# Performance work log

Hardware: AMD Instinct MI355X
Metric: run time of the kernel (lower is better)

Reference implementation:

```python
import jax, jax.numpy as jnp
from jax import lax
import numpy as np

B = 1048576       # batched program states
L = 64            # hidden width of LinearNNComplex
STEPS = 19        # While test: state[5] < var(19), step counter +1 per iter


def setup_inputs() -> dict:
    key = jax.random.key(0)
    ks = jax.random.split(key, 7)
    x = jax.random.normal(ks[0], (B, 6), dtype=jnp.float32)
    x = x.at[:, 5].set(0.0)  # step counter starts at 0 so the While runs 19 iters
    # LinearNNComplex params: Linear(2,L) -> ReLU -> Linear(L,L) -> ReLU -> Linear(L,3) -> Sigmoid
    s1 = 1.0 / np.sqrt(2.0)
    s2 = 1.0 / np.sqrt(float(L))
    W1 = jax.random.normal(ks[1], (2, L), dtype=jnp.float32) * s1
    b1 = jax.random.normal(ks[2], (L,), dtype=jnp.float32) * s1
    W2 = jax.random.normal(ks[3], (L, L), dtype=jnp.float32) * s2
    b2 = jax.random.normal(ks[4], (L,), dtype=jnp.float32) * s2
    W3 = jax.random.normal(ks[5], (L, 3), dtype=jnp.float32) * s2
    b3 = jax.random.normal(ks[6], (3,), dtype=jnp.float32) * s2
    return {"x": x, "W1": W1, "b1": b1, "W2": W2, "b2": b2, "W3": W3, "b3": b3}


def reference(x, W1, b1, W2, b2, W3, b3):
    """Batched Program interpreter.

    State columns: [0]=position, [1]=forward counter, [2:5]=branch probs,
    [5]=step counter. Each iteration:
      state[2:5] = sigmoid-MLP(state[0:2])            (assign_branch_probability)
      argmax over cols 2,3,4 picks branch:            (argmax_p)
        0 -> move_up    (col0 -= 1)
        1 -> move_right (col0 unchanged)
        2 -> move_down  (col0 += 1)
      state[1] += 1                                   (forward_update)
      state[5] += 1                                   (step_update)
    Runs STEPS=19 iterations (While: state[5] < 19).
    """
    def nn(z):  # z: [B, 2]
        h = jax.nn.relu(z @ W1 + b1)
        h = jax.nn.relu(h @ W2 + b2)
        return jax.nn.sigmoid(h @ W3 + b3)  # [B, 3]

    def body(state, _):
        p = nn(state[:, :2])                         # [B, 3]
        idx = jnp.argmax(p, axis=-1)                 # [B]
        delta = (idx - 1).astype(state.dtype)        # up=-1, right=0, down=+1
        new = jnp.concatenate(
            [
                (state[:, 0] + delta)[:, None],
                (state[:, 1] + 1.0)[:, None],
                p,
                (state[:, 5] + 1.0)[:, None],
            ],
            axis=-1,
        )
        return new, None

    final, _ = lax.scan(body, x, None, length=STEPS)
    return final  # [B, 6]
```

## Files before the change

kernel.cpp:

```cpp
#include <hip/hip_runtime.h>
#include <math.h>


#define NSTEPS 19

typedef _Float16 half8   __attribute__((ext_vector_type(8)));
typedef _Float16 half2v  __attribute__((ext_vector_type(2)));
typedef float    float2v __attribute__((ext_vector_type(2)));
typedef float    float4v __attribute__((ext_vector_type(4)));

__device__ __forceinline__ half2v pkrtz(float a, float b) {
    return __builtin_bit_cast(half2v, __builtin_amdgcn_cvt_pkrtz(a, b));
}
__device__ __forceinline__ float swz_xor16(float v) {
    int r = __builtin_amdgcn_ds_swizzle(__builtin_bit_cast(int, v), 0x401F);
    return __builtin_bit_cast(float, r);
}
__device__ __forceinline__ float2v lo2(float4v v) {
    return __builtin_shufflevector(v, v, 0, 1);
}
__device__ __forceinline__ float2v hi2(float4v v) {
    return __builtin_shufflevector(v, v, 2, 3);
}

__global__ __launch_bounds__(256, 2)
void program_kernel(const float* __restrict__ x,
                    const float* __restrict__ W1,
                    const float* __restrict__ b1,
                    const float* __restrict__ W2,
                    const float* __restrict__ b2,
                    const float* __restrict__ W3,
                    const float* __restrict__ b3,
                    float* __restrict__ out,
                    int B) {
    const int tid    = threadIdx.x;
    const int lane   = tid & 63;
    const int wave   = tid >> 6;
    const int lanelo = lane & 15;
    const int q8     = lane >> 4;
    const int myRow  = blockIdx.x * 64 + wave * 16 + lanelo;
    const int rowLd  = myRow < B ? myRow : (B - 1);

    float2v w1a[8], w1b[8], b1v[8];
    #pragma unroll
    for (int kf = 0; kf < 2; ++kf) {
        const int k0 = kf * 32 + q8 * 8;
        const float2v* a = (const float2v*)(W1 + k0);
        const float2v* bb = (const float2v*)(W1 + 64 + k0);
        const float2v* bv = (const float2v*)(b1 + k0);
        #pragma unroll
        for (int i = 0; i < 4; ++i) {
            w1a[kf * 4 + i] = a[i];
            w1b[kf * 4 + i] = bb[i];
            b1v[kf * 4 + i] = bv[i];
        }
    }

    half8 Wh[2][4], Wl[2][4];
    #pragma unroll
    for (int kf = 0; kf < 2; ++kf) {
        #pragma unroll
        for (int t = 0; t < 4; ++t) {
            half8 bh, bl;
            #pragma unroll
            for (int j = 0; j < 8; ++j) {
                const float w =
                    W2[(kf * 32 + q8 * 8 + j) * 64 + t * 16 + lanelo];
                const _Float16 wh = (_Float16)w;
                const _Float16 wl = (_Float16)((w - (float)wh) * 4096.0f);
                bh[j] = wh;
                bl[j] = wl;
            }
            Wh[kf][t] = bh;
            Wl[kf][t] = bl;
        }
    }

    float4v b2f[4];
    #pragma unroll
    for (int t = 0; t < 4; ++t) {
        const int n = t * 16 + q8 * 4;
        b2f[t] = (float4v){b2[n], b2[n + 1], b2[n + 2], b2[n + 3]};
    }

    float2v d10[8], d20[8];
    #pragma unroll
    for (int p = 0; p < 8; ++p) {
        const int n0 = (p >> 1) * 16 + q8 * 4 + (p & 1) * 2;
        const float w00 = W3[n0 * 3 + 0],       w01 = W3[n0 * 3 + 1];
        const float w02 = W3[n0 * 3 + 2];
        const float w10 = W3[(n0 + 1) * 3 + 0], w11 = W3[(n0 + 1) * 3 + 1];
        const float w12 = W3[(n0 + 1) * 3 + 2];
        d10[p] = (float2v){w01 - w00, w11 - w10};
        d20[p] = (float2v){w02 - w00, w12 - w10};
    }
    const float b3v0 = b3[0];
    const float db10 = b3[1] - b3[0];
    const float db20 = b3[2] - b3[0];

    float pos, fwd, c5;
    {
        const float* xr = x + (size_t)rowLd * 6;
        pos = xr[0];
        fwd = xr[1];
        c5  = xr[5];
    }

    const float4v zf = {0.f, 0.f, 0.f, 0.f};
    const float2v z2 = {0.f, 0.f};
    const float2v kinv = {1.0f / 4096.0f, 1.0f / 4096.0f};
    float l0 = 0.f, l1 = 0.f, l2 = 0.f;

    #pragma unroll 1
    for (int step = 0; step < NSTEPS; ++step) {
        const float2v posp = {pos, pos}, fwdp = {fwd, fwd};
        half8 Hh[2], Hl[2];
        #pragma unroll
        for (int kf = 0; kf < 2; ++kf) {
            union { half8 v; half2v h2[4]; } uh, ul;
            #pragma unroll
            for (int p = 0; p < 4; ++p) {
                const int e = kf * 4 + p;
                float2v z = __builtin_elementwise_fma(fwdp, w1b[e], b1v[e]);
                z = __builtin_elementwise_fma(posp, w1a[e], z);
                const float2v hp = __builtin_elementwise_max(z, z2);
                uh.h2[p] = pkrtz(hp[0], hp[1]);
                const float r0 = fmaf((float)uh.h2[p][0], -1.0f, hp[0]);
                const float r1 = fmaf((float)uh.h2[p][1], -1.0f, hp[1]);
                const float2v rp = (float2v){r0, r1} * 4096.0f;
                ul.h2[p] = pkrtz(rp[0], rp[1]);
            }
            Hh[kf] = uh.v;
            Hl[kf] = ul.v;
        }

        float4v accA[4], accB[4];
        #pragma unroll
        for (int t = 0; t < 4; ++t) {
            accB[t] = __builtin_amdgcn_mfma_f32_16x16x32_f16(
                Wl[0][t], Hh[0], zf, 0, 0, 0);
            accB[t] = __builtin_amdgcn_mfma_f32_16x16x32_f16(
                Wh[0][t], Hl[0], accB[t], 0, 0, 0);
            accB[t] = __builtin_amdgcn_mfma_f32_16x16x32_f16(
                Wl[1][t], Hh[1], accB[t], 0, 0, 0);
            accB[t] = __builtin_amdgcn_mfma_f32_16x16x32_f16(
                Wh[1][t], Hl[1], accB[t], 0, 0, 0);
            accA[t] = __builtin_amdgcn_mfma_f32_16x16x32_f16(
                Wh[0][t], Hh[0], b2f[t], 0, 0, 0);
            accA[t] = __builtin_amdgcn_mfma_f32_16x16x32_f16(
                Wh[1][t], Hh[1], accA[t], 0, 0, 0);
        }

        float2v h2p[8];
        #pragma unroll
        for (int t = 0; t < 4; ++t) {
            h2p[2 * t] = __builtin_elementwise_max(
                __builtin_elementwise_fma(lo2(accB[t]), kinv, lo2(accA[t])),
                z2);
            h2p[2 * t + 1] = __builtin_elementwise_max(
                __builtin_elementwise_fma(hi2(accB[t]), kinv, hi2(accA[t])),
                z2);
        }

        float2v s1 = z2, s2 = z2;
        #pragma unroll
        for (int p = 0; p < 8; ++p) {
            s1 = __builtin_elementwise_fma(h2p[p], d10[p], s1);
            s2 = __builtin_elementwise_fma(h2p[p], d20[p], s2);
        }
        float g10 = s1[0] + s1[1];
        float g20 = s2[0] + s2[1];
        g10 += swz_xor16(g10);
        g20 += swz_xor16(g20);
        g10 += __shfl_xor(g10, 32, 64);
        g20 += __shfl_xor(g20, 32, 64);
        g10 += db10;
        g20 += db20;

        if (step == NSTEPS - 1) {
            float2v s0 = z2;
            #pragma unroll
            for (int p = 0; p < 8; ++p) {
                const int n0 = (p >> 1) * 16 + q8 * 4 + (p & 1) * 2;
                const float2v w30 = {W3[n0 * 3], W3[(n0 + 1) * 3]};
                s0 = __builtin_elementwise_fma(h2p[p], w30, s0);
            }
            float t0 = s0[0] + s0[1];
            t0 += swz_xor16(t0);
            t0 += __shfl_xor(t0, 32, 64);
            l0 = t0 + b3v0;
            l1 = l0 + g10;
            l2 = l0 + g20;
        }

        const float delta =
            (g20 > fmaxf(0.f, g10)) ? 1.0f : ((g10 > 0.f) ? 0.0f : -1.0f);
        pos += delta;
        fwd += 1.0f;
    }

    if (q8 == 0 && myRow < B) {
        const float p0 = 1.f / (1.f + __expf(-l0));
        const float p1 = 1.f / (1.f + __expf(-l1));
        const float p2 = 1.f / (1.f + __expf(-l2));
        float2* o = (float2*)(out + (size_t)myRow * 6);
        o[0] = make_float2(pos, fwd);
        o[1] = make_float2(p0, p1);
        o[2] = make_float2(p2, c5 + (float)NSTEPS);
    }
}

extern "C" void kernel_launch(void* const* d_in, const int* in_sizes, int n_in,
                              void* d_out, int out_size, void* d_ws, size_t ws_size,
                              hipStream_t stream) {
    const float* x  = (const float*)d_in[0];
    const float* W1 = (const float*)d_in[1];
    const float* b1 = (const float*)d_in[2];
    const float* W2 = (const float*)d_in[3];
    const float* b2 = (const float*)d_in[4];
    const float* W3 = (const float*)d_in[5];
    const float* b3 = (const float*)d_in[6];
    float* out = (float*)d_out;

    const int B = in_sizes[0] / 6;
    const int nBlocks = (B + 63) / 64;

    program_kernel<<<nBlocks, 256, 0, stream>>>(
        x, W1, b1, W2, b2, W3, b3, out, B);
}
```

Baseline: 632.6 us.

## Process three 16-row tiles per wave to amortize register-resident weights

Each wave now handles three independent 16-row sub-tiles instead of one, reusing the register-held split-fp16 W2 fragments and layer-1/layer-3 constants across them. Blocks shrink to a single wave and the grid is resized. This cuts the per-row cost of the weight setup and gives the scheduler independent MFMA chains to interleave. In exchange it raises register pressure, which may lower occupancy, and it changes the block shape.

Result: slower. 801.8 us (+26.7%).

```diff
diff --git a/kernel.cpp b/kernel.cpp
--- a/kernel.cpp
+++ b/kernel.cpp
@@ -3,6 +3,7 @@
 
 
 #define NSTEPS 19
+#define NS 3
 
 typedef _Float16 half8   __attribute__((ext_vector_type(8)));
 typedef _Float16 half2v  __attribute__((ext_vector_type(2)));
@@ -23,7 +24,7 @@
     return __builtin_shufflevector(v, v, 2, 3);
 }
 
-__global__ __launch_bounds__(256, 2)
+__global__ __launch_bounds__(64, 1)
 void program_kernel(const float* __restrict__ x,
                     const float* __restrict__ W1,
                     const float* __restrict__ b1,
@@ -33,13 +34,16 @@
                     const float* __restrict__ b3,
                     float* __restrict__ out,
                     int B) {
-    const int tid    = threadIdx.x;
-    const int lane   = tid & 63;
-    const int wave   = tid >> 6;
+    const int lane   = threadIdx.x & 63;
     const int lanelo = lane & 15;
     const int q8     = lane >> 4;
-    const int myRow  = blockIdx.x * 64 + wave * 16 + lanelo;
-    const int rowLd  = myRow < B ? myRow : (B - 1);
+
+    int myRow[NS], rowLd[NS];
+    #pragma unroll
+    for (int S = 0; S < NS; ++S) {
+        myRow[S] = blockIdx.x * (16 * NS) + S * 16 + lanelo;
+        rowLd[S] = myRow[S] < B ? myRow[S] : (B - 1);
+    }
 
     float2v w1a[8], w1b[8], b1v[8];
     #pragma unroll
@@ -98,115 +102,132 @@
     const float db10 = b3[1] - b3[0];
     const float db20 = b3[2] - b3[0];
 
-    float pos, fwd, c5;
-    {
-        const float* xr = x + (size_t)rowLd * 6;
-        pos = xr[0];
-        fwd = xr[1];
-        c5  = xr[5];
+    float pos[NS], fwd[NS], c5[NS];
+    #pragma unroll
+    for (int S = 0; S < NS; ++S) {
+        const float* xr = x + (size_t)rowLd[S] * 6;
+        pos[S] = xr[0];
+        fwd[S] = xr[1];
+        c5[S]  = xr[5];
     }
 
     const float4v zf = {0.f, 0.f, 0.f, 0.f};
     const float2v z2 = {0.f, 0.f};
     const float2v kinv = {1.0f / 4096.0f, 1.0f / 4096.0f};
-    float l0 = 0.f, l1 = 0.f, l2 = 0.f;
+    float l0[NS], l1[NS], l2[NS];
+    #pragma unroll
+    for (int S = 0; S < NS; ++S) { l0[S] = l1[S] = l2[S] = 0.f; }
 
     #pragma unroll 1
     for (int step = 0; step < NSTEPS; ++step) {
-        const float2v posp = {pos, pos}, fwdp = {fwd, fwd};
-        half8 Hh[2], Hl[2];
-        #pragma unroll
-        for (int kf = 0; kf < 2; ++kf) {
-            union { half8 v; half2v h2[4]; } uh, ul;
-            #pragma unroll
-            for (int p = 0; p < 4; ++p) {
-                const int e = kf * 4 + p;
-                float2v z = __builtin_elementwise_fma(fwdp, w1b[e], b1v[e]);
-                z = __builtin_elementwise_fma(posp, w1a[e], z);
-                const float2v hp = __builtin_elementwise_max(z, z2);
-                uh.h2[p] = pkrtz(hp[0], hp[1]);
-                const float r0 = fmaf((float)uh.h2[p][0], -1.0f, hp[0]);
-                const float r1 = fmaf((float)uh.h2[p][1], -1.0f, hp[1]);
-                const float2v rp = (float2v){r0, r1} * 4096.0f;
-                ul.h2[p] = pkrtz(rp[0], rp[1]);
-            }
-            Hh[kf] = uh.v;
-            Hl[kf] = ul.v;
-        }
-
-        float4v accA[4], accB[4];
-        #pragma unroll
-        for (int t = 0; t < 4; ++t) {
-            accB[t] = __builtin_amdgcn_mfma_f32_16x16x32_f16(
-                Wl[0][t], Hh[0], zf, 0, 0, 0);
-            accB[t] = __builtin_amdgcn_mfma_f32_16x16x32_f16(
-                Wh[0][t], Hl[0], accB[t], 0, 0, 0);
-            accB[t] = __builtin_amdgcn_mfma_f32_16x16x32_f16(
-                Wl[1][t], Hh[1], accB[t], 0, 0, 0);
-            accB[t] = __builtin_amdgcn_mfma_f32_16x16x32_f16(
-                Wh[1][t], Hl[1], accB[t], 0, 0, 0);
-            accA[t] = __builtin_amdgcn_mfma_f32_16x16x32_f16(
-                Wh[0][t], Hh[0], b2f[t], 0, 0, 0);
-            accA[t] = __builtin_amdgcn_mfma_f32_16x16x32_f16(
-                Wh[1][t], Hh[1], accA[t], 0, 0, 0);
-        }
-
-        float2v h2p[8];
-        #pragma unroll
-        for (int t = 0; t < 4; ++t) {
-            h2p[2 * t] = __builtin_elementwise_max(
-                __builtin_elementwise_fma(lo2(accB[t]), kinv, lo2(accA[t])),
-                z2);
-            h2p[2 * t + 1] = __builtin_elementwise_max(
-                __builtin_elementwise_fma(hi2(accB[t]), kinv, hi2(accA[t])),
-                z2);
-        }
-
-        float2v s1 = z2, s2 = z2;
-        #pragma unroll
-        for (int p = 0; p < 8; ++p) {
-            s1 = __builtin_elementwise_fma(h2p[p], d10[p], s1);
-            s2 = __builtin_elementwise_fma(h2p[p], d20[p], s2);
-        }
-        float g10 = s1[0] + s1[1];
-        float g20 = s2[0] + s2[1];
-        g10 += swz_xor16(g10);
-        g20 += swz_xor16(g20);
-        g10 += __shfl_xor(g10, 32, 64);
-        g20 += __shfl_xor(g20, 32, 64);
-        g10 += db10;
-        g20 += db20;
-
-        if (step == NSTEPS - 1) {
-            float2v s0 = z2;
+        half8 Hh[NS][2], Hl[NS][2];
+        #pragma unroll
+        for (int S = 0; S < NS; ++S) {
+            const float2v posp = {pos[S], pos[S]}, fwdp = {fwd[S], fwd[S]};
+            #pragma unroll
+            for (int kf = 0; kf < 2; ++kf) {
+                union { half8 v; half2v h2[4]; } uh, ul;
+                #pragma unroll
+                for (int p = 0; p < 4; ++p) {
+                    const int e = kf * 4 + p;
+                    float2v z = __builtin_elementwise_fma(fwdp, w1b[e], b1v[e]);
+                    z = __builtin_elementwise_fma(posp, w1a[e], z);
+                    const float2v hp = __builtin_elementwise_max(z, z2);
+                    uh.h2[p] = pkrtz(hp[0], hp[1]);
+                    const float r0 = fmaf((float)uh.h2[p][0], -1.0f, hp[0]);
+                    const float r1 = fmaf((float)uh.h2[p][1], -1.0f, hp[1]);
+                    const float2v rp = (float2v){r0, r1} * 4096.0f;
+                    ul.h2[p] = pkrtz(rp[0], rp[1]);
+                }
+                Hh[S][kf] = uh.v;
+                Hl[S][kf] = ul.v;
+            }
+        }
+
+        float4v accA[NS][4], accB[NS][4];
+        #pragma unroll
+        for (int S = 0; S < NS; ++S) {
+            #pragma unroll
+            for (int t = 0; t < 4; ++t) {
+                accB[S][t] = __builtin_amdgcn_mfma_f32_16x16x32_f16(
+                    Wl[0][t], Hh[S][0], zf, 0, 0, 0);
+                accB[S][t] = __builtin_amdgcn_mfma_f32_16x16x32_f16(
+                    Wh[0][t], Hl[S][0], accB[S][t], 0, 0, 0);
+                accB[S][t] = __builtin_amdgcn_mfma_f32_16x16x32_f16(
+                    Wl[1][t], Hh[S][1], accB[S][t], 0, 0, 0);
+                accB[S][t] = __builtin_amdgcn_mfma_f32_16x16x32_f16(
+                    Wh[1][t], Hl[S][1], accB[S][t], 0, 0, 0);
+                accA[S][t] = __builtin_amdgcn_mfma_f32_16x16x32_f16(
+                    Wh[0][t], Hh[S][0], b2f[t], 0, 0, 0);
+                accA[S][t] = __builtin_amdgcn_mfma_f32_16x16x32_f16(
+                    Wh[1][t], Hh[S][1], accA[S][t], 0, 0, 0);
+            }
+        }
+
+        #pragma unroll
+        for (int S = 0; S < NS; ++S) {
+            float2v h2p[8];
+            #pragma unroll
+            for (int t = 0; t < 4; ++t) {
+                h2p[2 * t] = __builtin_elementwise_max(
+                    __builtin_elementwise_fma(lo2(accB[S][t]), kinv,
+                                              lo2(accA[S][t])),
+                    z2);
+                h2p[2 * t + 1] = __builtin_elementwise_max(
+                    __builtin_elementwise_fma(hi2(accB[S][t]), kinv,
+                                              hi2(accA[S][t])),
+                    z2);
+            }
+
+            float2v s1 = z2, s2 = z2;
             #pragma unroll
             for (int p = 0; p < 8; ++p) {
-                const int n0 = (p >> 1) * 16 + q8 * 4 + (p & 1) * 2;
-                const float2v w30 = {W3[n0 * 3], W3[(n0 + 1) * 3]};
-                s0 = __builtin_elementwise_fma(h2p[p], w30, s0);
-            }
-            float t0 = s0[0] + s0[1];
-            t0 += swz_xor16(t0);
-            t0 += __shfl_xor(t0, 32, 64);
-            l0 = t0 + b3v0;
-            l1 = l0 + g10;
-            l2 = l0 + g20;
-        }
-
-        const float delta =
-            (g20 > fmaxf(0.f, g10)) ? 1.0f : ((g10 > 0.f) ? 0.0f : -1.0f);
-        pos += delta;
-        fwd += 1.0f;
-    }
-
-    if (q8 == 0 && myRow < B) {
-        const float p0 = 1.f / (1.f + __expf(-l0));
-        const float p1 = 1.f / (1.f + __expf(-l1));
-        const float p2 = 1.f / (1.f + __expf(-l2));
-        float2* o = (float2*)(out + (size_t)myRow * 6);
-        o[0] = make_float2(pos, fwd);
-        o[1] = make_float2(p0, p1);
-        o[2] = make_float2(p2, c5 + (float)NSTEPS);
+                s1 = __builtin_elementwise_fma(h2p[p], d10[p], s1);
+                s2 = __builtin_elementwise_fma(h2p[p], d20[p], s2);
+            }
+            float g10 = s1[0] + s1[1];
+            float g20 = s2[0] + s2[1];
+            g10 += swz_xor16(g10);
+            g20 += swz_xor16(g20);
+            g10 += __shfl_xor(g10, 32, 64);
+            g20 += __shfl_xor(g20, 32, 64);
+            g10 += db10;
+            g20 += db20;
+
+            if (step == NSTEPS - 1) {
+                float2v s0 = z2;
+                #pragma unroll
+                for (int p = 0; p < 8; ++p) {
+                    const int n0 = (p >> 1) * 16 + q8 * 4 + (p & 1) * 2;
+                    const float2v w30 = {W3[n0 * 3], W3[(n0 + 1) * 3]};
+                    s0 = __builtin_elementwise_fma(h2p[p], w30, s0);
+                }
+                float t0 = s0[0] + s0[1];
+                t0 += swz_xor16(t0);
+                t0 += __shfl_xor(t0, 32, 64);
+                l0[S] = t0 + b3v0;
+                l1[S] = l0[S] + g10;
+                l2[S] = l0[S] + g20;
+            }
+
+            const float delta =
+                (g20 > fmaxf(0.f, g10)) ? 1.0f : ((g10 > 0.f) ? 0.0f : -1.0f);
+            pos[S] += delta;
+            fwd[S] += 1.0f;
+        }
+    }
+
+    #pragma unroll
+    for (int S = 0; S < NS; ++S) {
+        if (q8 == 0 && myRow[S] < B) {
+            const float p0 = 1.f / (1.f + __expf(-l0[S]));
+            const float p1 = 1.f / (1.f + __expf(-l1[S]));
+            const float p2 = 1.f / (1.f + __expf(-l2[S]));
+            float2* o = (float2*)(out + (size_t)myRow[S] * 6);
+            o[0] = make_float2(pos[S], fwd[S]);
+            o[1] = make_float2(p0, p1);
+            o[2] = make_float2(p2, c5[S] + (float)NSTEPS);
+        }
     }
 }
 
@@ -223,8 +244,9 @@
     float* out = (float*)d_out;
 
     const int B = in_sizes[0] / 6;
-    const int nBlocks = (B + 63) / 64;
-
-    program_kernel<<<nBlocks, 256, 0, stream>>>(
+    const int rowsPerBlock = 16 * NS;
+    const int nBlocks = (B + rowsPerBlock - 1) / rowsPerBlock;
+
+    program_kernel<<<nBlocks, 64, 0, stream>>>(
         x, W1, b1, W2, b2, W3, b3, out, B);
 }
```

## Stage W2 fragments and layer-3 weights in LDS to raise occupancy

Applied to the files above, without the earlier changes.

Wave 0 now converts W2 into split fp16 hi/lo fragments, prepares the b2 and W3-difference constants once per block, and stores them all in shared memory. Each step reloads these fragments from LDS instead of holding them in registers, and launch bounds are raised from 2 to 3 blocks per SIMD. The aim is to cut VGPR pressure so more waves can hide MFMA and ALU latency. The cost is extra LDS reads inside every loop iteration plus a block barrier, and the MFMA sequence is reordered into two k-halves so loads can overlap with compute.

Result: slower. 1.741 ms (+175.1%).

```diff
diff --git a/kernel.cpp b/kernel.cpp
--- a/kernel.cpp
+++ b/kernel.cpp
@@ -23,7 +23,7 @@
     return __builtin_shufflevector(v, v, 2, 3);
 }
 
-__global__ __launch_bounds__(256, 2)
+__global__ __launch_bounds__(256, 3)
 void program_kernel(const float* __restrict__ x,
                     const float* __restrict__ W1,
                     const float* __restrict__ b1,
@@ -33,6 +33,10 @@
                     const float* __restrict__ b3,
                     float* __restrict__ out,
                     int B) {
+    __shared__ half8   ldsW[2][2][4][4][16];
+    __shared__ float4v ldsB2f[4][4];
+    __shared__ float2v ldsD[2][8][4];
+
     const int tid    = threadIdx.x;
     const int lane   = tid & 63;
     const int wave   = tid >> 6;
@@ -56,44 +60,43 @@
         }
     }
 
-    half8 Wh[2][4], Wl[2][4];
-    #pragma unroll
-    for (int kf = 0; kf < 2; ++kf) {
-        #pragma unroll
-        for (int t = 0; t < 4; ++t) {
-            half8 bh, bl;
+    if (wave == 0) {
+        #pragma unroll
+        for (int kf = 0; kf < 2; ++kf) {
             #pragma unroll
-            for (int j = 0; j < 8; ++j) {
-                const float w =
-                    W2[(kf * 32 + q8 * 8 + j) * 64 + t * 16 + lanelo];
-                const _Float16 wh = (_Float16)w;
-                const _Float16 wl = (_Float16)((w - (float)wh) * 4096.0f);
-                bh[j] = wh;
-                bl[j] = wl;
+            for (int t = 0; t < 4; ++t) {
+                half8 bh, bl;
+                #pragma unroll
+                for (int j = 0; j < 8; ++j) {
+                    const float w =
+                        W2[(kf * 32 + q8 * 8 + j) * 64 + t * 16 + lanelo];
+                    const _Float16 wh = (_Float16)w;
+                    const _Float16 wl = (_Float16)((w - (float)wh) * 4096.0f);
+                    bh[j] = wh;
+                    bl[j] = wl;
+                }
+                ldsW[0][kf][t][q8][lanelo] = bh;
+                ldsW[1][kf][t][q8][lanelo] = bl;
             }
-            Wh[kf][t] = bh;
-            Wl[kf][t] = bl;
-        }
-    }
-
-    float4v b2f[4];
-    #pragma unroll
-    for (int t = 0; t < 4; ++t) {
-        const int n = t * 16 + q8 * 4;
-        b2f[t] = (float4v){b2[n], b2[n + 1], b2[n + 2], b2[n + 3]};
-    }
-
-    float2v d10[8], d20[8];
-    #pragma unroll
-    for (int p = 0; p < 8; ++p) {
-        const int n0 = (p >> 1) * 16 + q8 * 4 + (p & 1) * 2;
-        const float w00 = W3[n0 * 3 + 0],       w01 = W3[n0 * 3 + 1];
-        const float w02 = W3[n0 * 3 + 2];
-        const float w10 = W3[(n0 + 1) * 3 + 0], w11 = W3[(n0 + 1) * 3 + 1];
-        const float w12 = W3[(n0 + 1) * 3 + 2];
-        d10[p] = (float2v){w01 - w00, w11 - w10};
-        d20[p] = (float2v){w02 - w00, w12 - w10};
-    }
+        }
+        if (lane < 16) {
+            const int t = lane >> 2, q = lane & 3;
+            const int n = t * 16 + q * 4;
+            ldsB2f[t][q] = (float4v){b2[n], b2[n + 1], b2[n + 2], b2[n + 3]};
+        }
+        if (lane < 32) {
+            const int p = lane >> 2, q = lane & 3;
+            const int n0 = (p >> 1) * 16 + q * 4 + (p & 1) * 2;
+            const float w00 = W3[n0 * 3 + 0],       w01 = W3[n0 * 3 + 1];
+            const float w02 = W3[n0 * 3 + 2];
+            const float w10 = W3[(n0 + 1) * 3 + 0], w11 = W3[(n0 + 1) * 3 + 1];
+            const float w12 = W3[(n0 + 1) * 3 + 2];
+            ldsD[0][p][q] = (float2v){w01 - w00, w11 - w10};
+            ldsD[1][p][q] = (float2v){w02 - w00, w12 - w10};
+        }
+    }
+    __syncthreads();
+
     const float b3v0 = b3[0];
     const float db10 = b3[1] - b3[0];
     const float db20 = b3[2] - b3[0];
@@ -113,6 +116,15 @@
 
     #pragma unroll 1
     for (int step = 0; step < NSTEPS; ++step) {
+        half8 wh0[4], wl0[4];
+        float4v b2r[4];
+        #pragma unroll
+        for (int t = 0; t < 4; ++t) {
+            wh0[t] = ldsW[0][0][t][q8][lanelo];
+            wl0[t] = ldsW[1][0][t][q8][lanelo];
+            b2r[t] = ldsB2f[t][q8];
+        }
+
         const float2v posp = {pos, pos}, fwdp = {fwd, fwd};
         half8 Hh[2], Hl[2];
         #pragma unroll
@@ -138,17 +150,27 @@
         #pragma unroll
         for (int t = 0; t < 4; ++t) {
             accB[t] = __builtin_amdgcn_mfma_f32_16x16x32_f16(
-                Wl[0][t], Hh[0], zf, 0, 0, 0);
-            accB[t] = __builtin_amdgcn_mfma_f32_16x16x32_f16(
-                Wh[0][t], Hl[0], accB[t], 0, 0, 0);
-            accB[t] = __builtin_amdgcn_mfma_f32_16x16x32_f16(
-                Wl[1][t], Hh[1], accB[t], 0, 0, 0);
-            accB[t] = __builtin_amdgcn_mfma_f32_16x16x32_f16(
-                Wh[1][t], Hl[1], accB[t], 0, 0, 0);
+                wl0[t], Hh[0], zf, 0, 0, 0);
+            accB[t] = __builtin_amdgcn_mfma_f32_16x16x32_f16(
+                wh0[t], Hl[0], accB[t], 0, 0, 0);
             accA[t] = __builtin_amdgcn_mfma_f32_16x16x32_f16(
-                Wh[0][t], Hh[0], b2f[t], 0, 0, 0);
+                wh0[t], Hh[0], b2r[t], 0, 0, 0);
+        }
+
+        half8 wh1[4], wl1[4];
+        #pragma unroll
+        for (int t = 0; t < 4; ++t) {
+            wh1[t] = ldsW[0][1][t][q8][lanelo];
+            wl1[t] = ldsW[1][1][t][q8][lanelo];
+        }
+        #pragma unroll
+        for (int t = 0; t < 4; ++t) {
+            accB[t] = __builtin_amdgcn_mfma_f32_16x16x32_f16(
+                wl1[t], Hh[1], accB[t], 0, 0, 0);
+            accB[t] = __builtin_amdgcn_mfma_f32_16x16x32_f16(
+                wh1[t], Hl[1], accB[t], 0, 0, 0);
             accA[t] = __builtin_amdgcn_mfma_f32_16x16x32_f16(
-                Wh[1][t], Hh[1], accA[t], 0, 0, 0);
+                wh1[t], Hh[1], accA[t], 0, 0, 0);
         }
 
         float2v h2p[8];
@@ -162,11 +184,17 @@
                 z2);
         }
 
+        float2v d10r[8], d20r[8];
+        #pragma unroll
+        for (int p = 0; p < 8; ++p) {
+            d10r[p] = ldsD[0][p][q8];
+            d20r[p] = ldsD[1][p][q8];
+        }
         float2v s1 = z2, s2 = z2;
         #pragma unroll
         for (int p = 0; p < 8; ++p) {
-            s1 = __builtin_elementwise_fma(h2p[p], d10[p], s1);
-            s2 = __builtin_elementwise_fma(h2p[p], d20[p], s2);
+            s1 = __builtin_elementwise_fma(h2p[p], d10r[p], s1);
+            s2 = __builtin_elementwise_fma(h2p[p], d20r[p], s2);
         }
         float g10 = s1[0] + s1[1];
         float g20 = s2[0] + s2[1];
```
